# Performance work log

Hardware: AMD Instinct MI355X
Metric: run time of the kernel (lower is better)

The kernel has to match this reference:

```python
import jax, jax.numpy as jnp
from jax import lax
import numpy as np

B, L, E, H = 4, 512, 1024, 128


def setup_inputs() -> dict:
    key = jax.random.key(0)
    k0, k1, k2, k3, k4, k5 = jax.random.split(key, 6)
    s = 1.0 / np.sqrt(E)
    return {
        "rec_emb": jax.random.normal(k0, (B, L, E), jnp.float32),
        "lig_emb": jax.random.normal(k1, (B, L, E), jnp.float32),
        "W1": jax.random.normal(k2, (E, H), jnp.float32) * s,
        "b1": jax.random.normal(k3, (H,), jnp.float32) * 0.01,
        "conv_w": jax.random.normal(k4, (1, H, 2, 2), jnp.float32) * (1.0 / np.sqrt(H * 4)),
        "conv_b": jax.random.normal(k5, (1,), jnp.float32) * 0.01,
    }


def reference(rec_emb, lig_emb, W1, b1, conv_w, conv_b):
    # shared fc: Linear -> ReLU (Dropout is identity in eval mode)
    rec_hid = jax.nn.relu(jnp.einsum("bie,eh->bih", rec_emb, W1) + b1)
    lig_hid = jax.nn.relu(jnp.einsum("bje,eh->bjh", lig_emb, W1) + b1)
    # outer-product bilinear map: bih,bjh->bijh, then tanh
    mat = jnp.tanh(rec_hid[:, :, None, :] * lig_hid[:, None, :, :])
    # permute to NCHW: (b, h, i, j)
    mat = jnp.transpose(mat, (0, 3, 1, 2))
    # Conv2d(H -> 1, kernel=2, padding=1): out spatial = L + 1
    y = lax.conv_general_dilated(
        mat, conv_w, window_strides=(1, 1), padding=[(1, 1), (1, 1)],
        dimension_numbers=("NCHW", "OIHW", "NCHW"),
    ) + conv_b[None, :, None, None]
    # MaxPool2d(kernel=2, stride=2), floor mode
    pooled = lax.reduce_window(
        y, -jnp.inf, lax.max,
        window_dimensions=(1, 1, 2, 2), window_strides=(1, 1, 2, 2),
        padding="VALID",
    )
    # global max over spatial dims -> (b, 1), sigmoid, flatten
    m = jnp.max(pooled, axis=(2, 3))
    return jax.nn.sigmoid(m).reshape(-1)
```

## Files before the change

kernel.cpp:

```cpp
#include <hip/hip_runtime.h>
#include <hip/hip_fp16.h>
#include <math.h>

#define BDIM 4
#define LDIM 512
#define EDIM 1024
#define HDIM 128
#define TILE 32
#define NT   16
#define K2   2.885390081777927f

typedef unsigned short ushort_t;
typedef __attribute__((ext_vector_type(8))) _Float16 half8;
typedef __attribute__((ext_vector_type(4))) float f32x4;

struct __align__(16) H8 { __half2 p[4]; };
union HU { H8 h; half8 v; };

__global__ __launch_bounds__(256) void gemm_direct(
    const float* __restrict__ rec, const float* __restrict__ lig,
    const float* __restrict__ W1, const float* __restrict__ b1,
    const float* __restrict__ cw, ushort_t* __restrict__ hid,
    ushort_t* __restrict__ wneg, float* __restrict__ wsumg) {
  if (blockIdx.x == 512) {
    __shared__ float wp[2][4];
    const int t = threadIdx.x;
    if (t < HDIM) {
      float4 w4 = *(const float4*)&cw[t * 4];
      _Float16 h0 = (_Float16)(-2.f * w4.x), h1 = (_Float16)(-2.f * w4.y);
      _Float16 h2 = (_Float16)(-2.f * w4.z), h3 = (_Float16)(-2.f * w4.w);
      wneg[0 * HDIM + t] = *(ushort_t*)&h0;
      wneg[1 * HDIM + t] = *(ushort_t*)&h1;
      wneg[2 * HDIM + t] = *(ushort_t*)&h2;
      wneg[3 * HDIM + t] = *(ushort_t*)&h3;
#pragma unroll
      for (int k = 4; k < 16; ++k) wneg[k * HDIM + t] = 0;
      float4 ws = w4;
#pragma unroll
      for (int off = 32; off > 0; off >>= 1) {
        ws.x += __shfl_down(ws.x, off, 64);
        ws.y += __shfl_down(ws.y, off, 64);
        ws.z += __shfl_down(ws.z, off, 64);
        ws.w += __shfl_down(ws.w, off, 64);
      }
      if ((t & 63) == 0) {
        wp[t >> 6][0] = ws.x; wp[t >> 6][1] = ws.y;
        wp[t >> 6][2] = ws.z; wp[t >> 6][3] = ws.w;
      }
    }
    __syncthreads();
    if (t < 4) wsumg[t] = wp[0][t] + wp[1][t];
    return;
  }

  const int gw = (int)blockIdx.x * 4 + (threadIdx.x >> 6);
  const int l = threadIdx.x & 63;
  const int strip = gw >> 3;
  const int nidx = gw & 7;
  const int r0 = strip * 16;
  const int m = l & 15, q = l >> 4;
  const float* arow = ((r0 < BDIM * LDIM)
                           ? rec + (size_t)r0 * EDIM
                           : lig + (size_t)(r0 - BDIM * LDIM) * EDIM) +
                      (size_t)m * EDIM + q * 8;
  const int col = nidx * 16 + m;
  const float* wcol = W1 + col;

  f32x4 acc = {0.f, 0.f, 0.f, 0.f};
  for (int blk = 0; blk < 8; ++blk) {
    float4 alo[4], ahi[4];
    float bw[4][8];
#pragma unroll
    for (int j = 0; j < 4; ++j) {
      const int k0 = (blk * 4 + j) * 32 + q * 8;
      alo[j] = *(const float4*)(arow + (blk * 4 + j) * 32);
      ahi[j] = *(const float4*)(arow + (blk * 4 + j) * 32 + 4);
#pragma unroll
      for (int kk = 0; kk < 8; ++kk)
        bw[j][kk] = wcol[(size_t)(k0 + kk) * HDIM];
    }
#pragma unroll
    for (int j = 0; j < 4; ++j) {
      HU au, bu;
      au.h.p[0] = __floats2half2_rn(alo[j].x, alo[j].y);
      au.h.p[1] = __floats2half2_rn(alo[j].z, alo[j].w);
      au.h.p[2] = __floats2half2_rn(ahi[j].x, ahi[j].y);
      au.h.p[3] = __floats2half2_rn(ahi[j].z, ahi[j].w);
      bu.h.p[0] = __floats2half2_rn(bw[j][0], bw[j][1]);
      bu.h.p[1] = __floats2half2_rn(bw[j][2], bw[j][3]);
      bu.h.p[2] = __floats2half2_rn(bw[j][4], bw[j][5]);
      bu.h.p[3] = __floats2half2_rn(bw[j][6], bw[j][7]);
      acc = __builtin_amdgcn_mfma_f32_16x16x32_f16(au.v, bu.v, acc, 0, 0, 0);
    }
  }
  const float scale = (r0 < BDIM * LDIM) ? -K2 : 1.0f;
  const float bias = b1[col];
#pragma unroll
  for (int r = 0; r < 4; ++r) {
    float v = fmaxf(acc[r] + bias, 0.f) * scale;
    ((_Float16*)hid)[(size_t)(r0 + q * 4 + r) * HDIM + col] = (_Float16)v;
  }
}

__global__ __launch_bounds__(256, 4) void bilinear_max(
    const ushort_t* __restrict__ hid, const ushort_t* __restrict__ wneg,
    const float* __restrict__ wsumg, const float* __restrict__ cw,
    const float* __restrict__ cb, float* __restrict__ partial) {
  __shared__ ushort_t rl[33][130];
  __shared__ ushort_t ll[33][130];
  __shared__ ushort_t sl4[33][34][4];
  __shared__ float wred[4];

  const int t = threadIdx.x;
  const int b = blockIdx.z;
  const int ib = (int)blockIdx.y * TILE - 1;
  const int jb = (int)blockIdx.x * TILE - 1;
  const int w = t >> 6, l = t & 63;
  const int q = l >> 4, c15 = l & 15;

  half8 wf[4];
#pragma unroll
  for (int c = 0; c < 4; ++c)
    wf[c] = *(const half8*)&wneg[c15 * HDIM + c * 32 + q * 8];
  const float wsum_v = (c15 < 4) ? wsumg[c15] : 0.f;

  H8 z;
  z.p[0] = z.p[1] = z.p[2] = z.p[3] = __floats2half2_rn(0.f, 0.f);
  for (int p = t; p < 66 * 16; p += 256) {
    int r = p >> 4, seg = (p & 15) * 8;
    if (r < 33) {
      int i = ib + r;
      H8 v = z;
      if (i >= 0) v = *(const H8*)&hid[((size_t)(b * LDIM + i)) * HDIM + seg];
      *(H8*)&rl[r][seg] = v;
    } else {
      int j = jb + (r - 33);
      H8 v = z;
      if (j >= 0) v = *(const H8*)&hid[((size_t)((BDIM + b) * LDIM + j)) * HDIM + seg];
      *(H8*)&ll[r - 33][seg] = v;
    }
  }
  __syncthreads();

  const __half2 D0 = __float2half2_rn(0.998539f);
  const __half2 D1 = __float2half2_rn(-0.947090f);
  const __half2 D2 = __float2half2_rn(0.676154f);
  const __half2 D3 = __float2half2_rn(-0.228646f);
#define POLYG(U) \
  __hmul2(U, __hfma2(U, __hfma2(U, __hfma2(U, D3, D2), D1), D0))
#define GCHAIN(GU, RU, LU)                                                    \
  {                                                                           \
    __half2 u0 = h2exp2(__hmul2((RU).h.p[0], (LU).h.p[0]));                   \
    __half2 u1 = h2exp2(__hmul2((RU).h.p[1], (LU).h.p[1]));                   \
    __half2 u2 = h2exp2(__hmul2((RU).h.p[2], (LU).h.p[2]));                   \
    __half2 u3 = h2exp2(__hmul2((RU).h.p[3], (LU).h.p[3]));                   \
    (GU).h.p[0] = POLYG(u0);                                                  \
    (GU).h.p[1] = POLYG(u1);                                                  \
    (GU).h.p[2] = POLYG(u2);                                                  \
    (GU).h.p[3] = POLYG(u3);                                                  \
  }

#pragma unroll
  for (int hf = 0; hf < 2; ++hf) {
    const int jj0 = hf << 4;
    HU lu[4];
#pragma unroll
    for (int c = 0; c < 4; ++c)
      lu[c].v = *(const half8*)&ll[jj0 + c15][c * 32 + q * 8];
    for (int ii2 = 0; ii2 < 4; ++ii2) {
      const int iiA = w * 8 + ii2 * 2, iiB = iiA + 1;
      HU ruA[4], ruB[4];
#pragma unroll
      for (int c = 0; c < 4; ++c) {
        ruA[c].v = *(const half8*)&rl[iiA][c * 32 + q * 8];
        ruB[c].v = *(const half8*)&rl[iiB][c * 32 + q * 8];
      }
      f32x4 accA = {0.f, 0.f, 0.f, 0.f}, accB = {0.f, 0.f, 0.f, 0.f};
#pragma unroll
      for (int c = 0; c < 4; ++c) {
        HU gA, gB;
        GCHAIN(gA, ruA[c], lu[c])
        GCHAIN(gB, ruB[c], lu[c])
        accA = __builtin_amdgcn_mfma_f32_16x16x32_f16(gA.v, wf[c], accA, 0, 0, 0);
        accB = __builtin_amdgcn_mfma_f32_16x16x32_f16(gB.v, wf[c], accB, 0, 0, 0);
      }
      if (c15 < 4) {
#pragma unroll
        for (int r = 0; r < 4; ++r) {
          _Float16 ha = (_Float16)(wsum_v + accA[r]);
          _Float16 hb = (_Float16)(wsum_v + accB[r]);
          sl4[iiA][jj0 + q * 4 + r][c15] = *(ushort_t*)&ha;
          sl4[iiB][jj0 + q * 4 + r][c15] = *(ushort_t*)&hb;
        }
      }
    }
  }
#undef GCHAIN

  if (t < 130) {
    const int pr = t >> 1;
    const int hh = (t & 1) * 64;
    const int pi = (pr < 33) ? pr : 32;
    const int qj = (pr < 33) ? 32 : (pr - 33);
    float sa0 = 0.f, sa1 = 0.f, sa2 = 0.f, sa3 = 0.f;
    for (int h8 = hh; h8 < hh + 64; h8 += 8) {
      HU r8, l8;
      r8.v = *(const half8*)&rl[pi][h8];
      l8.v = *(const half8*)&ll[qj][h8];
#pragma unroll
      for (int j = 0; j < 4; ++j) {
        float2 pf = __half22float2(__hmul2(r8.h.p[j], l8.h.p[j]));
        float u0 = __builtin_amdgcn_exp2f(pf.x);
        float u1 = __builtin_amdgcn_exp2f(pf.y);
        float g0 = u0 * fmaf(u0, fmaf(u0, fmaf(u0, -0.228646f, 0.676154f), -0.947090f), 0.998539f);
        float g1 = u1 * fmaf(u1, fmaf(u1, fmaf(u1, -0.228646f, 0.676154f), -0.947090f), 0.998539f);
        float4 wa = *(const float4*)&cw[(h8 + 2 * j) * 4];
        float4 wb = *(const float4*)&cw[(h8 + 2 * j + 1) * 4];
        sa0 = fmaf(-2.f * g0, wa.x, fmaf(-2.f * g1, wb.x, sa0));
        sa1 = fmaf(-2.f * g0, wa.y, fmaf(-2.f * g1, wb.y, sa1));
        sa2 = fmaf(-2.f * g0, wa.z, fmaf(-2.f * g1, wb.z, sa2));
        sa3 = fmaf(-2.f * g0, wa.w, fmaf(-2.f * g1, wb.w, sa3));
      }
    }
    sa0 += __shfl_xor(sa0, 1, 64);
    sa1 += __shfl_xor(sa1, 1, 64);
    sa2 += __shfl_xor(sa2, 1, 64);
    sa3 += __shfl_xor(sa3, 1, 64);
    if ((t & 1) == 0) {
      _Float16 h0 = (_Float16)(wsumg[0] + sa0);
      _Float16 h1 = (_Float16)(wsumg[1] + sa1);
      _Float16 h2 = (_Float16)(wsumg[2] + sa2);
      _Float16 h3 = (_Float16)(wsumg[3] + sa3);
      sl4[pi][qj][0] = *(ushort_t*)&h0;
      sl4[pi][qj][1] = *(ushort_t*)&h1;
      sl4[pi][qj][2] = *(ushort_t*)&h2;
      sl4[pi][qj][3] = *(ushort_t*)&h3;
    }
  }
  __syncthreads();

  float m = -INFINITY;
  const float cbv = cb[0];
  for (int p = t; p < 1024; p += 256) {
    int jj = (p & 31) + 1, iy = (p >> 5) + 1;
    float v = cbv + (float)(*(const _Float16*)&sl4[iy - 1][jj - 1][0])
                  + (float)(*(const _Float16*)&sl4[iy - 1][jj][1])
                  + (float)(*(const _Float16*)&sl4[iy][jj - 1][2])
                  + (float)(*(const _Float16*)&sl4[iy][jj][3]);
    m = fmaxf(m, v);
  }
#pragma unroll
  for (int off = 32; off > 0; off >>= 1) m = fmaxf(m, __shfl_down(m, off, 64));
  if ((t & 63) == 0) wred[t >> 6] = m;
  __syncthreads();
  if (t == 0) {
    float mm = fmaxf(fmaxf(wred[0], wred[1]), fmaxf(wred[2], wred[3]));
    partial[((size_t)b * NT + blockIdx.y) * NT + blockIdx.x] = mm;
  }
}

__global__ __launch_bounds__(64) void finalize(const float* __restrict__ partial,
                                               float* __restrict__ out) {
  const int b = blockIdx.x, t = threadIdx.x;
  float m = -INFINITY;
  for (int p = t; p < NT * NT; p += 64) m = fmaxf(m, partial[b * NT * NT + p]);
#pragma unroll
  for (int off = 32; off > 0; off >>= 1) m = fmaxf(m, __shfl_down(m, off, 64));
  if (t == 0) out[b] = 1.f / (1.f + expf(-m));
}

extern "C" void kernel_launch(void* const* d_in, const int* in_sizes, int n_in,
                              void* d_out, int out_size, void* d_ws, size_t ws_size,
                              hipStream_t stream) {
  const float* rec = (const float*)d_in[0];
  const float* lig = (const float*)d_in[1];
  const float* W1  = (const float*)d_in[2];
  const float* b1  = (const float*)d_in[3];
  const float* cw  = (const float*)d_in[4];
  const float* cb  = (const float*)d_in[5];
  float* out = (float*)d_out;

  ushort_t* hid  = (ushort_t*)d_ws;
  float* partial = (float*)(hid + (size_t)2 * BDIM * LDIM * HDIM);
  ushort_t* wneg = (ushort_t*)(partial + NT * NT * BDIM);
  float* wsumg   = (float*)(wneg + 16 * HDIM);

  gemm_direct<<<dim3(513), 256, 0, stream>>>(rec, lig, W1, b1, cw, hid, wneg, wsumg);
  bilinear_max<<<dim3(NT, NT, BDIM), 256, 0, stream>>>(hid, wneg, wsumg, cw, cb, partial);
  finalize<<<dim3(BDIM), 64, 0, stream>>>(partial, out);
}
```

Measured before the change: 123.8 us.

## Lower tanh polynomial degree and process four rows per unrolled MFMA pass

```diff
diff --git a/kernel.cpp b/kernel.cpp
--- a/kernel.cpp
+++ b/kernel.cpp
@@ -142,12 +142,10 @@
   }
   __syncthreads();
 
-  const __half2 D0 = __float2half2_rn(0.998539f);
-  const __half2 D1 = __float2half2_rn(-0.947090f);
-  const __half2 D2 = __float2half2_rn(0.676154f);
-  const __half2 D3 = __float2half2_rn(-0.228646f);
-#define POLYG(U) \
-  __hmul2(U, __hfma2(U, __hfma2(U, __hfma2(U, D3, D2), D1), D0))
+  const __half2 E0 = __float2half2_rn(0.991381f);
+  const __half2 E1 = __float2half2_rn(-0.818328f);
+  const __half2 E2 = __float2half2_rn(0.333048f);
+#define POLYG(U) __hmul2(U, __hfma2(U, __hfma2(U, E2, E1), E0))
 #define GCHAIN(GU, RU, LU)                                                    \
   {                                                                           \
     __half2 u0 = h2exp2(__hmul2((RU).h.p[0], (LU).h.p[0]));                   \
@@ -167,30 +165,37 @@
 #pragma unroll
     for (int c = 0; c < 4; ++c)
       lu[c].v = *(const half8*)&ll[jj0 + c15][c * 32 + q * 8];
-    for (int ii2 = 0; ii2 < 4; ++ii2) {
-      const int iiA = w * 8 + ii2 * 2, iiB = iiA + 1;
-      HU ruA[4], ruB[4];
+#pragma unroll
+    for (int ii4 = 0; ii4 < 2; ++ii4) {
+      const int ii = w * 8 + ii4 * 4;
+      f32x4 a0 = {0.f, 0.f, 0.f, 0.f}, a1 = a0, a2 = a0, a3 = a0;
 #pragma unroll
       for (int c = 0; c < 4; ++c) {
-        ruA[c].v = *(const half8*)&rl[iiA][c * 32 + q * 8];
-        ruB[c].v = *(const half8*)&rl[iiB][c * 32 + q * 8];
-      }
-      f32x4 accA = {0.f, 0.f, 0.f, 0.f}, accB = {0.f, 0.f, 0.f, 0.f};
-#pragma unroll
-      for (int c = 0; c < 4; ++c) {
-        HU gA, gB;
-        GCHAIN(gA, ruA[c], lu[c])
-        GCHAIN(gB, ruB[c], lu[c])
-        accA = __builtin_amdgcn_mfma_f32_16x16x32_f16(gA.v, wf[c], accA, 0, 0, 0);
-        accB = __builtin_amdgcn_mfma_f32_16x16x32_f16(gB.v, wf[c], accB, 0, 0, 0);
+        HU r0, r1, r2, r3, g0, g1, g2, g3;
+        r0.v = *(const half8*)&rl[ii + 0][c * 32 + q * 8];
+        r1.v = *(const half8*)&rl[ii + 1][c * 32 + q * 8];
+        r2.v = *(const half8*)&rl[ii + 2][c * 32 + q * 8];
+        r3.v = *(const half8*)&rl[ii + 3][c * 32 + q * 8];
+        GCHAIN(g0, r0, lu[c])
+        GCHAIN(g1, r1, lu[c])
+        GCHAIN(g2, r2, lu[c])
+        GCHAIN(g3, r3, lu[c])
+        a0 = __builtin_amdgcn_mfma_f32_16x16x32_f16(g0.v, wf[c], a0, 0, 0, 0);
+        a1 = __builtin_amdgcn_mfma_f32_16x16x32_f16(g1.v, wf[c], a1, 0, 0, 0);
+        a2 = __builtin_amdgcn_mfma_f32_16x16x32_f16(g2.v, wf[c], a2, 0, 0, 0);
+        a3 = __builtin_amdgcn_mfma_f32_16x16x32_f16(g3.v, wf[c], a3, 0, 0, 0);
       }
       if (c15 < 4) {
 #pragma unroll
         for (int r = 0; r < 4; ++r) {
-          _Float16 ha = (_Float16)(wsum_v + accA[r]);
-          _Float16 hb = (_Float16)(wsum_v + accB[r]);
-          sl4[iiA][jj0 + q * 4 + r][c15] = *(ushort_t*)&ha;
-          sl4[iiB][jj0 + q * 4 + r][c15] = *(ushort_t*)&hb;
+          _Float16 h0 = (_Float16)(wsum_v + a0[r]);
+          _Float16 h1 = (_Float16)(wsum_v + a1[r]);
+          _Float16 h2 = (_Float16)(wsum_v + a2[r]);
+          _Float16 h3 = (_Float16)(wsum_v + a3[r]);
+          sl4[ii + 0][jj0 + q * 4 + r][c15] = *(ushort_t*)&h0;
+          sl4[ii + 1][jj0 + q * 4 + r][c15] = *(ushort_t*)&h1;
+          sl4[ii + 2][jj0 + q * 4 + r][c15] = *(ushort_t*)&h2;
+          sl4[ii + 3][jj0 + q * 4 + r][c15] = *(ushort_t*)&h3;
         }
       }
     }
@@ -212,8 +217,8 @@
         float2 pf = __half22float2(__hmul2(r8.h.p[j], l8.h.p[j]));
         float u0 = __builtin_amdgcn_exp2f(pf.x);
         float u1 = __builtin_amdgcn_exp2f(pf.y);
-        float g0 = u0 * fmaf(u0, fmaf(u0, fmaf(u0, -0.228646f, 0.676154f), -0.947090f), 0.998539f);
-        float g1 = u1 * fmaf(u1, fmaf(u1, fmaf(u1, -0.228646f, 0.676154f), -0.947090f), 0.998539f);
+        float g0 = u0 * fmaf(u0, fmaf(u0, 0.333048f, -0.818328f), 0.991381f);
+        float g1 = u1 * fmaf(u1, fmaf(u1, 0.333048f, -0.818328f), 0.991381f);
         float4 wa = *(const float4*)&cw[(h8 + 2 * j) * 4];
         float4 wb = *(const float4*)&cw[(h8 + 2 * j + 1) * 4];
         sa0 = fmaf(-2.f * g0, wa.x, fmaf(-2.f * g1, wb.x, sa0));
```

Measured after the change: 122.7 us. No clear change (-0.9%).
